# Performance work log

Measured on AMD Instinct MI355X. Metric: run time of the kernel, lower is better.

## Reference

```python
import jax, jax.numpy as jnp
import numpy as np

N = 8192
IN_C = 512
OUT_C = 512


def setup_inputs() -> dict:
    key = jax.random.key(0)
    k1, k2, k3 = jax.random.split(key, 3)
    x = jax.random.normal(k1, (N, IN_C), dtype=jnp.float32)
    adj = jax.random.uniform(k2, (N, N), dtype=jnp.float32)
    # torch.rand initializer for the weight (uniform [0,1))
    w = jax.random.uniform(k3, (IN_C, OUT_C), dtype=jnp.float32)
    return {"x": x, "adj": adj, "w": w}


def reference(x, adj, w):
    # A = adj + I
    A = adj + jnp.eye(adj.shape[0], dtype=adj.dtype)
    # D_hat = diag(deg)^{-1/2}; diagonal inverse + sqrt == elementwise rsqrt of degrees
    deg = jnp.sum(A, axis=1)                      # [N]
    d_inv_sqrt = jax.lax.rsqrt(deg)               # [N]
    # A_hat = D_hat @ A @ D_hat == row/col scaling (same math, no dense inverse)
    A_hat = A * d_inv_sqrt[:, None] * d_inv_sqrt[None, :]
    mm_1 = A_hat @ x                              # [N, in_c]
    return jax.nn.elu(mm_1 @ w)                   # [N, out_c]
```

## Files before the change

kernel.cpp:

```cpp
#include <hip/hip_runtime.h>

#define NN 8192
#define CC 512

typedef __attribute__((ext_vector_type(8))) short short8;
typedef __attribute__((ext_vector_type(4))) float f32x4;
typedef unsigned short ushort_t;

__device__ __forceinline__ unsigned short f2bf(float f) {
    unsigned int u = __float_as_uint(f);
    u += 0x7FFF + ((u >> 16) & 1);
    return (unsigned short)(u >> 16);
}

__device__ __forceinline__ void gload_lds16(const void* g, void* l) {
    __builtin_amdgcn_global_load_lds((const __attribute__((address_space(1))) unsigned int*)g,
                                     (__attribute__((address_space(3))) unsigned int*)l,
                                     16, 0, 0);
}

__global__ __launch_bounds__(256) void k_rowsum_cvt(const float* __restrict__ adj,
                                                    float* __restrict__ ds,
                                                    ushort_t* __restrict__ adj16) {
    int row = blockIdx.x;
    const float4* p = (const float4*)(adj + (size_t)row * NN);
    ushort4* q = (ushort4*)(adj16 + (size_t)row * NN);
    float s = 0.f;
#pragma unroll
    for (int i = 0; i < 8; ++i) {
        float4 v = p[threadIdx.x + i * 256];
        s += (v.x + v.y) + (v.z + v.w);
        ushort4 u;
        u.x = f2bf(v.x); u.y = f2bf(v.y); u.z = f2bf(v.z); u.w = f2bf(v.w);
        q[threadIdx.x + i * 256] = u;
    }
#pragma unroll
    for (int off = 32; off > 0; off >>= 1) s += __shfl_down(s, off, 64);
    __shared__ float partial[4];
    if ((threadIdx.x & 63) == 0) partial[threadIdx.x >> 6] = s;
    __syncthreads();
    if (threadIdx.x == 0) {
        float deg = ((partial[0] + partial[1]) + (partial[2] + partial[3])) + 1.0f;
        ds[row] = rsqrtf(deg);
    }
}

__global__ __launch_bounds__(256) void k_rowsum(const float* __restrict__ adj,
                                                float* __restrict__ ds) {
    int row = blockIdx.x;
    const float4* p = (const float4*)(adj + (size_t)row * NN);
    float s = 0.f;
#pragma unroll
    for (int i = 0; i < 8; ++i) {
        float4 v = p[threadIdx.x + i * 256];
        s += (v.x + v.y) + (v.z + v.w);
    }
#pragma unroll
    for (int off = 32; off > 0; off >>= 1) s += __shfl_down(s, off, 64);
    __shared__ float partial[4];
    if ((threadIdx.x & 63) == 0) partial[threadIdx.x >> 6] = s;
    __syncthreads();
    if (threadIdx.x == 0) {
        float deg = ((partial[0] + partial[1]) + (partial[2] + partial[3])) + 1.0f;
        ds[row] = rsqrtf(deg);
    }
}

__global__ __launch_bounds__(256) void k_transpose(const float* __restrict__ in,
                                                   ushort_t* __restrict__ out,
                                                   const float* __restrict__ scale,
                                                   int R, int C) {
    __shared__ float tile[64][65];
    int r0 = blockIdx.x * 64, c0 = blockIdx.y * 64;
    int t = threadIdx.x;
    int cl = t & 63;
    int rl0 = t >> 6;
#pragma unroll
    for (int i = 0; i < 16; ++i) {
        int r = rl0 + i * 4;
        float v = in[(size_t)(r0 + r) * C + c0 + cl];
        float sc = scale ? scale[r0 + r] : 1.0f;
        tile[r][cl] = v * sc;
    }
    __syncthreads();
#pragma unroll
    for (int i = 0; i < 16; ++i) {
        int c = rl0 + i * 4;
        int r = cl;
        out[(size_t)(c0 + c) * R + r0 + r] = f2bf(tile[r][c]);
    }
}

__global__ __launch_bounds__(512, 2) void k_gemm1c(const ushort_t* __restrict__ adj16,
                                                   const ushort_t* __restrict__ yt,
                                                   float* __restrict__ part) {
    __shared__ __align__(16) ushort_t As[2][256 * 32];
    __shared__ __align__(16) ushort_t Bs[2][256 * 32];

    int t = threadIdx.x;
    int wid = t >> 6, lane = t & 63;

    int gid = blockIdx.x;
    int xcd = gid & 7, slot = gid >> 3;
    int cb = slot & 1;
    int u = (slot >> 1) + 16 * xcd;
    int rb = u & 31, ks = u >> 5;
    int rowBase = rb * 256, colBase = cb * 256;
    int kt0 = ks * 64, ktN = kt0 + 64;

    int wr = wid >> 2, wc = wid & 3;
    int fr = lane & 15, fq = lane >> 4;

    int row0 = t >> 2, c0 = t & 3;
    int sw0 = (c0 ^ (row0 & 3)) << 3;
    const ushort_t* aSrc0 = adj16 + (size_t)(rowBase + row0) * NN + sw0;
    const ushort_t* aSrc1 = adj16 + (size_t)(rowBase + row0 + 128) * NN + sw0;
    const ushort_t* bSrc0 = yt + (size_t)(colBase + row0) * NN + sw0;
    const ushort_t* bSrc1 = yt + (size_t)(colBase + row0 + 128) * NN + sw0;

    auto stage = [&](int buf, int kt) {
        int ko = kt * 32;
        gload_lds16(aSrc0 + ko, (char*)As[buf] + wid * 1024);
        gload_lds16(aSrc1 + ko, (char*)As[buf] + 8192 + wid * 1024);
        gload_lds16(bSrc0 + ko, (char*)Bs[buf] + wid * 1024);
        gload_lds16(bSrc1 + ko, (char*)Bs[buf] + 8192 + wid * 1024);
    };

    f32x4 acc[8][4] = {};
    int sws = (fq ^ (fr & 3)) << 4;

    stage(0, kt0);
    __syncthreads();
    int cur = 0;
    for (int kt = kt0; kt < ktN; ++kt) {
        if (kt + 1 < ktN) stage(cur ^ 1, kt + 1);
        const char* Ab = (const char*)As[cur];
        const char* Bb = (const char*)Bs[cur];
        short8 af[8], bfr[4];
#pragma unroll
        for (int m = 0; m < 8; ++m) {
            int row = wr * 128 + m * 16 + fr;
            af[m] = *(const short8*)(Ab + row * 64 + sws);
        }
#pragma unroll
        for (int n = 0; n < 4; ++n) {
            int col = wc * 64 + n * 16 + fr;
            bfr[n] = *(const short8*)(Bb + col * 64 + sws);
        }
        __builtin_amdgcn_s_setprio(1);
#pragma unroll
        for (int m = 0; m < 8; ++m)
#pragma unroll
            for (int n = 0; n < 4; ++n)
                acc[m][n] = __builtin_amdgcn_mfma_f32_16x16x32_bf16(af[m], bfr[n], acc[m][n], 0, 0, 0);
        __builtin_amdgcn_s_setprio(0);
        __syncthreads();
        cur ^= 1;
    }

#pragma unroll
    for (int m = 0; m < 8; ++m) {
#pragma unroll
        for (int j = 0; j < 4; ++j) {
            int gr = rowBase + wr * 128 + m * 16 + fq * 4 + j;
            float* dst = &part[((size_t)ks * NN + gr) * CC];
#pragma unroll
            for (int n = 0; n < 4; ++n) {
                int gc = colBase + wc * 64 + n * 16 + fr;
                dst[gc] = acc[m][n][j];
            }
        }
    }
}

template <int MODE>
__global__ __launch_bounds__(256, 4) void k_gemm1(const float* __restrict__ adj,
                                                  const ushort_t* __restrict__ yt,
                                                  const float* __restrict__ ds,
                                                  const float* __restrict__ x,
                                                  ushort_t* __restrict__ mm1,
                                                  float* __restrict__ part) {
    __shared__ __align__(16) ushort_t As[128 * 64];
    __shared__ __align__(16) ushort_t Bs[128 * 64];

    int t = threadIdx.x;
    int wid = t >> 6, lane = t & 63;

    int rowBase, colBase, kt0, ktN, ks;
    if (MODE == 0) {
        int bid = blockIdx.x;
        bid = (bid & 7) * 32 + (bid >> 3);
        colBase = (bid & 3) * 128;
        rowBase = (bid >> 2) * 128;
        kt0 = 0; ktN = NN / 64; ks = 0;
    } else {
        int gid = blockIdx.x;
        int xcd = gid & 7, slot = gid >> 3;
        int cb = slot & 3;
        int g = (slot >> 2) * 8 + xcd;
        int rb = g & 63; ks = g >> 6;
        rowBase = rb * 128; colBase = cb * 128;
        kt0 = ks * (NN / 64 / 4); ktN = kt0 + NN / 64 / 4;
    }

    int ar = t >> 4;
    int ac4 = t & 15;
    const float* aptr = adj + (size_t)(rowBase + ar) * NN + ac4 * 4;
    int brow0 = t >> 3;
    int bs = t & 7;

    float4 areg[8];

    auto loadA = [&](int kt) {
        const float* p = aptr + kt * 64;
#pragma unroll
        for (int i = 0; i < 8; ++i)
            areg[i] = *(const float4*)(p + (size_t)i * 16 * NN);
    };
    auto writeA = [&]() {
#pragma unroll
        for (int i = 0; i < 8; ++i) {
            int row = i * 16 + ar;
            ushort4 u;
            u.x = f2bf(areg[i].x); u.y = f2bf(areg[i].y);
            u.z = f2bf(areg[i].z); u.w = f2bf(areg[i].w);
            *(ushort4*)((char*)As + row * 128 + ((ac4 * 8) ^ ((row & 7) << 4))) = u;
        }
    };
    auto stageB = [&](int kt) {
#pragma unroll
        for (int j = 0; j < 4; ++j) {
            int row = j * 32 + brow0;
            gload_lds16((const char*)(yt + (size_t)(colBase + row) * NN + kt * 64 +
                                      ((bs ^ (row & 7)) << 3)),
                        (char*)Bs + j * 4096 + wid * 1024);
        }
    };

    f32x4 acc[4][4] = {};
    int wr = wid >> 1, wc = wid & 1;
    int fr = lane & 15, fq = lane >> 4;

    loadA(kt0);
    for (int kt = kt0; kt < ktN; ++kt) {
        writeA();
        stageB(kt);
        __syncthreads();
        if (kt + 1 < ktN) loadA(kt + 1);
#pragma unroll
        for (int ks2 = 0; ks2 < 2; ++ks2) {
            short8 af[4], bf[4];
#pragma unroll
            for (int m = 0; m < 4; ++m) {
                int row = wr * 64 + m * 16 + fr;
                af[m] = *(const short8*)((const char*)As + row * 128 +
                                         ((ks2 * 64 + fq * 16) ^ ((row & 7) << 4)));
            }
#pragma unroll
            for (int n = 0; n < 4; ++n) {
                int col = wc * 64 + n * 16 + fr;
                bf[n] = *(const short8*)((const char*)Bs + col * 128 +
                                         ((ks2 * 64 + fq * 16) ^ ((col & 7) << 4)));
            }
#pragma unroll
            for (int m = 0; m < 4; ++m)
#pragma unroll
                for (int n = 0; n < 4; ++n)
                    acc[m][n] = __builtin_amdgcn_mfma_f32_16x16x32_bf16(af[m], bf[n], acc[m][n], 0, 0, 0);
        }
        __syncthreads();
    }

#pragma unroll
    for (int m = 0; m < 4; ++m) {
#pragma unroll
        for (int j = 0; j < 4; ++j) {
            int gr = rowBase + wr * 64 + m * 16 + fq * 4 + j;
            float dsr = (MODE == 0) ? ds[gr] : 0.f;
#pragma unroll
            for (int n = 0; n < 4; ++n) {
                int gc = colBase + wc * 64 + n * 16 + fr;
                float p = acc[m][n][j];
                if (MODE == 0) {
                    float v = dsr * (p + dsr * x[(size_t)gr * CC + gc]);
                    mm1[(size_t)gr * CC + gc] = f2bf(v);
                } else {
                    part[((size_t)ks * NN + gr) * CC + gc] = p;
                }
            }
        }
    }
}

__global__ __launch_bounds__(256) void k_finish(const float* __restrict__ part,
                                                const float* __restrict__ ds,
                                                const float* __restrict__ x,
                                                ushort_t* __restrict__ mm1,
                                                int nsplit) {
    size_t i = (size_t)blockIdx.x * 256 + threadIdx.x;
    const f32x4* p = (const f32x4*)part;
    const size_t stride = (size_t)NN * CC / 4;
    f32x4 s = p[i];
    for (int k = 1; k < nsplit; ++k) s += p[i + (size_t)k * stride];
    int row = (int)(i >> 7);
    float d = ds[row];
    f32x4 xv = ((const f32x4*)x)[i];
    ushort4 u;
    u.x = f2bf(d * (s[0] + d * xv[0]));
    u.y = f2bf(d * (s[1] + d * xv[1]));
    u.z = f2bf(d * (s[2] + d * xv[2]));
    u.w = f2bf(d * (s[3] + d * xv[3]));
    ((ushort4*)mm1)[i] = u;
}

__global__ __launch_bounds__(256, 2) void k_gemm2(const ushort_t* __restrict__ mm1,
                                                  const ushort_t* __restrict__ wt,
                                                  float* __restrict__ out) {
    __shared__ __align__(16) ushort_t As[128 * 64];
    __shared__ __align__(16) ushort_t Bs[128 * 64];

    int t = threadIdx.x;
    int wid = t >> 6, lane = t & 63;
    int bid = blockIdx.x;
    bid = (bid & 7) * 32 + (bid >> 3);
    int cb = bid & 3, rb = bid >> 2;
    int rowBase = rb * 128, colBase = cb * 128;

    int srow0 = t >> 3, ss = t & 7;

    f32x4 acc[4][4] = {};
    int wr = wid >> 1, wc = wid & 1;
    int fr = lane & 15, fq = lane >> 4;

    for (int kt = 0; kt < CC / 64; ++kt) {
#pragma unroll
        for (int j = 0; j < 4; ++j) {
            int row = j * 32 + srow0;
            gload_lds16((const char*)(mm1 + (size_t)(rowBase + row) * CC + kt * 64 +
                                      ((ss ^ (row & 7)) << 3)),
                        (char*)As + j * 4096 + wid * 1024);
            gload_lds16((const char*)(wt + (size_t)(colBase + row) * CC + kt * 64 +
                                      ((ss ^ (row & 7)) << 3)),
                        (char*)Bs + j * 4096 + wid * 1024);
        }
        __syncthreads();
#pragma unroll
        for (int ks = 0; ks < 2; ++ks) {
            short8 af[4], bf[4];
#pragma unroll
            for (int m = 0; m < 4; ++m) {
                int row = wr * 64 + m * 16 + fr;
                af[m] = *(const short8*)((const char*)As + row * 128 +
                                         ((ks * 64 + fq * 16) ^ ((row & 7) << 4)));
            }
#pragma unroll
            for (int n = 0; n < 4; ++n) {
                int col = wc * 64 + n * 16 + fr;
                bf[n] = *(const short8*)((const char*)Bs + col * 128 +
                                         ((ks * 64 + fq * 16) ^ ((col & 7) << 4)));
            }
#pragma unroll
            for (int m = 0; m < 4; ++m)
#pragma unroll
                for (int n = 0; n < 4; ++n)
                    acc[m][n] = __builtin_amdgcn_mfma_f32_16x16x32_bf16(af[m], bf[n], acc[m][n], 0, 0, 0);
        }
        __syncthreads();
    }

#pragma unroll
    for (int m = 0; m < 4; ++m) {
#pragma unroll
        for (int j = 0; j < 4; ++j) {
            int gr = rowBase + wr * 64 + m * 16 + fq * 4 + j;
#pragma unroll
            for (int n = 0; n < 4; ++n) {
                int gc = colBase + wc * 64 + n * 16 + fr;
                float v = acc[m][n][j];
                out[(size_t)gr * CC + gc] = v > 0.f ? v : expm1f(v);
            }
        }
    }
}

extern "C" void kernel_launch(void* const* d_in, const int* in_sizes, int n_in,
                              void* d_out, int out_size, void* d_ws, size_t ws_size,
                              hipStream_t stream) {
    const float* x   = (const float*)d_in[0];
    const float* adj = (const float*)d_in[1];
    const float* w   = (const float*)d_in[2];
    float* out = (float*)d_out;

    char* ws = (char*)d_ws;
    size_t off = 0;
    float*    ds  = (float*)(ws + off);  off += 32u << 10;
    ushort_t* yt  = (ushort_t*)(ws + off);  off += 8u << 20;
    ushort_t* wt  = (ushort_t*)(ws + off);  off += 512u << 10;
    ushort_t* mm1 = (ushort_t*)(ws + off);  off += 8u << 20;
    float*    part = (float*)(ws + off);
    const size_t partBytes = 4 * (size_t)NN * CC * 4;
    ushort_t* adj16 = (ushort_t*)(ws + off + partBytes);
    const size_t adjBytes = (size_t)NN * NN * 2;

    if (ws_size >= off + partBytes + adjBytes) {
        k_rowsum_cvt<<<NN, 256, 0, stream>>>(adj, ds, adj16);
        k_transpose<<<dim3(NN / 64, CC / 64), 256, 0, stream>>>(x, yt, ds, NN, CC);
        k_transpose<<<dim3(CC / 64, CC / 64), 256, 0, stream>>>(w, wt, nullptr, CC, CC);
        k_gemm1c<<<256, 512, 0, stream>>>(adj16, yt, part);
        k_finish<<<NN * CC / 4 / 256, 256, 0, stream>>>(part, ds, x, mm1, 4);
    } else if (ws_size >= off + partBytes) {
        k_rowsum<<<NN, 256, 0, stream>>>(adj, ds);
        k_transpose<<<dim3(NN / 64, CC / 64), 256, 0, stream>>>(x, yt, ds, NN, CC);
        k_transpose<<<dim3(CC / 64, CC / 64), 256, 0, stream>>>(w, wt, nullptr, CC, CC);
        k_gemm1<1><<<1024, 256, 0, stream>>>(adj, yt, ds, x, mm1, part);
        k_finish<<<NN * CC / 4 / 256, 256, 0, stream>>>(part, ds, x, mm1, 4);
    } else {
        k_rowsum<<<NN, 256, 0, stream>>>(adj, ds);
        k_transpose<<<dim3(NN / 64, CC / 64), 256, 0, stream>>>(x, yt, ds, NN, CC);
        k_transpose<<<dim3(CC / 64, CC / 64), 256, 0, stream>>>(w, wt, nullptr, CC, CC);
        k_gemm1<0><<<256, 256, 0, stream>>>(adj, yt, ds, x, mm1, part);
    }

    k_gemm2<<<256, 256, 0, stream>>>(mm1, wt, out);
}
```

Measured before the change: 229.9 us.

## Deepen GEMM LDS pipeline to four stages with explicit vmcnt waits

Moves the main adjacency GEMM from double-buffered to four-buffered LDS staging, keeping three tiles of global_load_lds in flight. Each iteration waits with a manual s_waitcnt vmcnt and raw s_barrier instead of __syncthreads. The LDS swizzle is also changed to XOR on (row>>1)&3, aimed at reducing bank conflicts. LDS use doubles to 128KB per block, which with launch_bounds(512,2) may limit occupancy. The wrap-around prefetch issues redundant loads at the tail.

```diff
diff --git a/kernel.cpp b/kernel.cpp
--- a/kernel.cpp
+++ b/kernel.cpp
@@ -94,8 +94,8 @@
 __global__ __launch_bounds__(512, 2) void k_gemm1c(const ushort_t* __restrict__ adj16,
                                                    const ushort_t* __restrict__ yt,
                                                    float* __restrict__ part) {
-    __shared__ __align__(16) ushort_t As[2][256 * 32];
-    __shared__ __align__(16) ushort_t Bs[2][256 * 32];
+    __shared__ __align__(16) ushort_t As[4][256 * 32];
+    __shared__ __align__(16) ushort_t Bs[4][256 * 32];
 
     int t = threadIdx.x;
     int wid = t >> 6, lane = t & 63;
@@ -106,13 +106,13 @@
     int u = (slot >> 1) + 16 * xcd;
     int rb = u & 31, ks = u >> 5;
     int rowBase = rb * 256, colBase = cb * 256;
-    int kt0 = ks * 64, ktN = kt0 + 64;
+    int kt0 = ks * 64;
 
     int wr = wid >> 2, wc = wid & 3;
     int fr = lane & 15, fq = lane >> 4;
 
     int row0 = t >> 2, c0 = t & 3;
-    int sw0 = (c0 ^ (row0 & 3)) << 3;
+    int sw0 = (c0 ^ ((row0 >> 1) & 3)) << 3;
     const ushort_t* aSrc0 = adj16 + (size_t)(rowBase + row0) * NN + sw0;
     const ushort_t* aSrc1 = adj16 + (size_t)(rowBase + row0 + 128) * NN + sw0;
     const ushort_t* bSrc0 = yt + (size_t)(colBase + row0) * NN + sw0;
@@ -127,26 +127,29 @@
     };
 
     f32x4 acc[8][4] = {};
-    int sws = (fq ^ (fr & 3)) << 4;
-
-    stage(0, kt0);
-    __syncthreads();
-    int cur = 0;
-    for (int kt = kt0; kt < ktN; ++kt) {
-        if (kt + 1 < ktN) stage(cur ^ 1, kt + 1);
-        const char* Ab = (const char*)As[cur];
-        const char* Bb = (const char*)Bs[cur];
+    int sws = (fq ^ ((fr >> 1) & 3)) << 4;
+
+    stage(0, kt0 + 0);
+    stage(1, kt0 + 1);
+    stage(2, kt0 + 2);
+
+    for (int j = 0; j < 64; ++j) {
+        stage((j + 3) & 3, kt0 + ((j + 3) & 63));
+        asm volatile("s_waitcnt vmcnt(12)" ::: "memory");
+        __builtin_amdgcn_sched_barrier(0);
+        __builtin_amdgcn_s_barrier();
+        __builtin_amdgcn_sched_barrier(0);
+
+        const char* Ab = (const char*)As[j & 3];
+        const char* Bb = (const char*)Bs[j & 3];
         short8 af[8], bfr[4];
 #pragma unroll
-        for (int m = 0; m < 8; ++m) {
-            int row = wr * 128 + m * 16 + fr;
-            af[m] = *(const short8*)(Ab + row * 64 + sws);
-        }
-#pragma unroll
-        for (int n = 0; n < 4; ++n) {
-            int col = wc * 64 + n * 16 + fr;
-            bfr[n] = *(const short8*)(Bb + col * 64 + sws);
-        }
+        for (int m = 0; m < 8; ++m)
+            af[m] = *(const short8*)(Ab + (wr * 128 + m * 16 + fr) * 64 + sws);
+#pragma unroll
+        for (int n = 0; n < 4; ++n)
+            bfr[n] = *(const short8*)(Bb + (wc * 64 + n * 16 + fr) * 64 + sws);
+
         __builtin_amdgcn_s_setprio(1);
 #pragma unroll
         for (int m = 0; m < 8; ++m)
@@ -154,8 +157,9 @@
             for (int n = 0; n < 4; ++n)
                 acc[m][n] = __builtin_amdgcn_mfma_f32_16x16x32_bf16(af[m], bfr[n], acc[m][n], 0, 0, 0);
         __builtin_amdgcn_s_setprio(0);
-        __syncthreads();
-        cur ^= 1;
+        __builtin_amdgcn_sched_barrier(0);
+        __builtin_amdgcn_s_barrier();
+        __builtin_amdgcn_sched_barrier(0);
     }
 
 #pragma unroll
```

Result: no change. 228.5 us (-0.6%).
